# Performance work log

Measured on AMD Instinct MI355X. Metric: run time of the kernel, lower is better.

Reference implementation:

```python
import jax, jax.numpy as jnp
import numpy as np


def setup_inputs() -> dict:
    key = jax.random.key(0)
    ks = jax.random.split(key, 5)
    b, f, h, w, c = 2, 16, 64, 64, 256
    heads, D = 8, 32
    hD = heads * D
    x = jax.random.normal(ks[0], (b, f, h, w, c), dtype=jnp.float32)
    s = 1.0 / np.sqrt(c)
    Wq = jax.random.normal(ks[1], (c, hD), dtype=jnp.float32) * s
    Wk = jax.random.normal(ks[2], (c, hD), dtype=jnp.float32) * s
    Wv = jax.random.normal(ks[3], (c, hD), dtype=jnp.float32) * s
    Wo = jax.random.normal(ks[4], (hD, c), dtype=jnp.float32) * s
    return {"x": x, "Wq": Wq, "Wk": Wk, "Wv": Wv, "Wo": Wo, "heads": heads}


def reference(x, Wq, Wk, Wv, Wo, heads):
    b, f, h, w, c = x.shape
    hD = Wq.shape[1]
    D = hD // heads
    n = h * w
    # fuse batch & frames; 1x1 conv == channel matmul
    xf = x.reshape(b * f, n, c)  # [(bf), n, c]

    def proj(W):
        # [(bf), n, hD] -> [(bf), heads, D, n]
        p = jnp.einsum('bnc,cd->bnd', xf, W)
        return p.reshape(b * f, n, heads, D).transpose(0, 2, 3, 1)

    q = jax.nn.softmax(proj(Wq), axis=-2)  # softmax over D (note: scale is dead code in source)
    k = jax.nn.softmax(proj(Wk), axis=-1)  # softmax over spatial n
    v = proj(Wv)
    context = jnp.einsum('bhdn,bhen->bhde', k, v)      # [(bf), heads, D, D]
    out = jnp.einsum('bhde,bhdn->bhen', context, q)    # [(bf), heads, D, n]
    out = out.transpose(0, 3, 1, 2).reshape(b * f, n, hD)
    out = jnp.einsum('bnd,dc->bnc', out, Wo)
    return out.reshape(b, f, h, w, c)
```

## Files before the change

kernel.cpp:

```cpp
#include <hip/hip_runtime.h>
#include <hip/hip_bf16.h>


typedef __attribute__((ext_vector_type(8))) short bf16x8;
typedef __attribute__((ext_vector_type(4))) float f32x4;

__device__ __forceinline__ unsigned short f2bf(float x) {
  __hip_bfloat16 h = __float2bfloat16(x);
  union { __hip_bfloat16 b; unsigned short u; } c; c.b = h; return c.u;
}

__device__ __forceinline__ void gl16(const unsigned short* g, unsigned short* l) {
  __builtin_amdgcn_global_load_lds((const __attribute__((address_space(1))) void*)g,
                                   (__attribute__((address_space(3))) void*)l, 16, 0, 0);
}

__global__ __launch_bounds__(256) void k0_prep(const float* __restrict__ Wq,
                                               const float* __restrict__ Wk,
                                               const float* __restrict__ Wv,
                                               unsigned short* __restrict__ WqT,
                                               unsigned short* __restrict__ WkvT) {
  int r = blockIdx.x, c = threadIdx.x;
  if (r < 256)      WqT [(r      )*256 + c] = f2bf(Wq[c*256 + r]);
  else if (r < 512) WkvT[(r - 256)*256 + c] = f2bf(Wk[c*256 + (r-256)]);
  else              WkvT[(r - 256)*256 + c] = f2bf(Wv[c*256 + (r-512)]);
}

__global__ __launch_bounds__(1024, 4) void k1w(const float* __restrict__ x,
                                               const unsigned short* __restrict__ WkvT,
                                               float* __restrict__ ctxp,
                                               unsigned short* __restrict__ XB) {
  __shared__ unsigned short As[2][32*256];
  __shared__ unsigned short slab[2][512*32];
  int bid = blockIdx.x;
  size_t rowbase = (size_t)bid * 256;
  int tid = threadIdx.x;
  int lane = tid & 63, w = tid >> 6;
  int cl = lane & 15, rq = (lane >> 4) << 2, fs = lane >> 4;
  int h = w & 7;
  bool isV = w >= 8;

  bf16x8 bfr[2][8];
#pragma unroll
  for (int ni = 0; ni < 2; ++ni)
#pragma unroll
    for (int kk = 0; kk < 8; ++kk)
      bfr[ni][kk] = *(const bf16x8*)(WkvT + (size_t)(w*32 + ni*16 + cl)*256 + kk*32 + fs*8);

  f32x4 c2[2] = {};
  float dena0 = 0.f, dena1 = 0.f;

  int ar = tid >> 5, as_ = tid & 31;
  int aw = ar*256 + ((as_ ^ (ar & 7)) << 3);
  const float* ap = x + (rowbase + ar)*256 + as_*8;
  unsigned short* xbp = XB + (rowbase + ar)*256 + as_*8;

  int ca0 = h*32 + cl, ca1 = h*32 + 16 + cl;
  int cb  = 256 + h*32 + (isV ? 16 : 0) + cl;
  int ra0 = ca0*32 + ((fs ^ ((ca0 ^ (ca0 >> 2)) & 3)) << 3);
  int ra1 = ca1*32 + ((fs ^ ((ca1 ^ (ca1 >> 2)) & 3)) << 3);
  int rb  = cb*32  + ((fs ^ ((cb  ^ (cb  >> 2)) & 3)) << 3);

  f32x4 acc[2][2];

  float4 pa0 = *(const float4*)ap;
  float4 pa1 = *(const float4*)(ap + 4);
  {
    unsigned short* Ab = &As[0][0];
    union { ushort4 u4[2]; int4 i4; } pk;
    pk.u4[0].x = f2bf(pa0.x); pk.u4[0].y = f2bf(pa0.y); pk.u4[0].z = f2bf(pa0.z); pk.u4[0].w = f2bf(pa0.w);
    pk.u4[1].x = f2bf(pa1.x); pk.u4[1].y = f2bf(pa1.y); pk.u4[1].z = f2bf(pa1.z); pk.u4[1].w = f2bf(pa1.w);
    *(int4*)(&Ab[aw]) = pk.i4;
    *(int4*)xbp = pk.i4;
  }
  {
    const float* apn = ap + 32*256;
    pa0 = *(const float4*)apn;
    pa1 = *(const float4*)(apn + 4);
  }
  __syncthreads();
  {
    unsigned short* Ab = &As[0][0];
#pragma unroll
    for (int m = 0; m < 2; ++m)
#pragma unroll
      for (int ni = 0; ni < 2; ++ni) acc[m][ni] = (f32x4){};
#pragma unroll
    for (int kk = 0; kk < 8; ++kk) {
      int so = (((kk*4 + fs) ^ (cl & 7)) << 3);
      bf16x8 a0 = *(const bf16x8*)(&Ab[cl*256 + so]);
      bf16x8 a1 = *(const bf16x8*)(&Ab[(16 + cl)*256 + so]);
#pragma unroll
      for (int ni = 0; ni < 2; ++ni) {
        acc[0][ni] = __builtin_amdgcn_mfma_f32_16x16x32_bf16(a0, bfr[ni][kk], acc[0][ni], 0, 0, 0);
        acc[1][ni] = __builtin_amdgcn_mfma_f32_16x16x32_bf16(a1, bfr[ni][kk], acc[1][ni], 0, 0, 0);
      }
    }
  }

  for (int t = 0; t < 7; ++t) {
    {
      unsigned short* sb = &slab[t & 1][0];
#pragma unroll
      for (int ni = 0; ni < 2; ++ni) {
        int c = w*32 + ni*16 + cl;
        int sw = (c ^ (c >> 2)) & 3;
#pragma unroll
        for (int m = 0; m < 2; ++m) {
          int n4 = m*16 + rq;
          ushort4 wv;
          if (!isV) {
            float e0 = __expf(acc[m][ni][0]), e1 = __expf(acc[m][ni][1]);
            float e2 = __expf(acc[m][ni][2]), e3 = __expf(acc[m][ni][3]);
            if (ni == 0) dena0 += (e0 + e1) + (e2 + e3); else dena1 += (e0 + e1) + (e2 + e3);
            wv.x = f2bf(e0); wv.y = f2bf(e1); wv.z = f2bf(e2); wv.w = f2bf(e3);
          } else {
            wv.x = f2bf(acc[m][ni][0]); wv.y = f2bf(acc[m][ni][1]);
            wv.z = f2bf(acc[m][ni][2]); wv.w = f2bf(acc[m][ni][3]);
          }
          *(ushort4*)(&sb[c*32 + (((n4 >> 3) ^ sw) << 3) + (n4 & 7)]) = wv;
        }
      }
    }
    {
      unsigned short* Ab = &As[(t + 1) & 1][0];
      union { ushort4 u4[2]; int4 i4; } pk;
      pk.u4[0].x = f2bf(pa0.x); pk.u4[0].y = f2bf(pa0.y); pk.u4[0].z = f2bf(pa0.z); pk.u4[0].w = f2bf(pa0.w);
      pk.u4[1].x = f2bf(pa1.x); pk.u4[1].y = f2bf(pa1.y); pk.u4[1].z = f2bf(pa1.z); pk.u4[1].w = f2bf(pa1.w);
      *(int4*)(&Ab[aw]) = pk.i4;
      *(int4*)(xbp + (size_t)(t + 1)*8192) = pk.i4;
    }
    if (t < 6) {
      const float* apn = ap + (size_t)(t + 2)*32*256;
      pa0 = *(const float4*)apn;
      pa1 = *(const float4*)(apn + 4);
    }
    __syncthreads();
    {
      unsigned short* sb = &slab[t & 1][0];
      bf16x8 af0 = *(const bf16x8*)(&sb[ra0]);
      bf16x8 af1 = *(const bf16x8*)(&sb[ra1]);
      bf16x8 bv  = *(const bf16x8*)(&sb[rb]);
      c2[0] = __builtin_amdgcn_mfma_f32_16x16x32_bf16(af0, bv, c2[0], 0, 0, 0);
      c2[1] = __builtin_amdgcn_mfma_f32_16x16x32_bf16(af1, bv, c2[1], 0, 0, 0);
    }
    {
      unsigned short* Ab = &As[(t + 1) & 1][0];
#pragma unroll
      for (int m = 0; m < 2; ++m)
#pragma unroll
        for (int ni = 0; ni < 2; ++ni) acc[m][ni] = (f32x4){};
#pragma unroll
      for (int kk = 0; kk < 8; ++kk) {
        int so = (((kk*4 + fs) ^ (cl & 7)) << 3);
        bf16x8 a0 = *(const bf16x8*)(&Ab[cl*256 + so]);
        bf16x8 a1 = *(const bf16x8*)(&Ab[(16 + cl)*256 + so]);
#pragma unroll
        for (int ni = 0; ni < 2; ++ni) {
          acc[0][ni] = __builtin_amdgcn_mfma_f32_16x16x32_bf16(a0, bfr[ni][kk], acc[0][ni], 0, 0, 0);
          acc[1][ni] = __builtin_amdgcn_mfma_f32_16x16x32_bf16(a1, bfr[ni][kk], acc[1][ni], 0, 0, 0);
        }
      }
    }
  }
  {
    unsigned short* sb = &slab[1][0];
#pragma unroll
    for (int ni = 0; ni < 2; ++ni) {
      int c = w*32 + ni*16 + cl;
      int sw = (c ^ (c >> 2)) & 3;
#pragma unroll
      for (int m = 0; m < 2; ++m) {
        int n4 = m*16 + rq;
        ushort4 wv;
        if (!isV) {
          float e0 = __expf(acc[m][ni][0]), e1 = __expf(acc[m][ni][1]);
          float e2 = __expf(acc[m][ni][2]), e3 = __expf(acc[m][ni][3]);
          if (ni == 0) dena0 += (e0 + e1) + (e2 + e3); else dena1 += (e0 + e1) + (e2 + e3);
          wv.x = f2bf(e0); wv.y = f2bf(e1); wv.z = f2bf(e2); wv.w = f2bf(e3);
        } else {
          wv.x = f2bf(acc[m][ni][0]); wv.y = f2bf(acc[m][ni][1]);
          wv.z = f2bf(acc[m][ni][2]); wv.w = f2bf(acc[m][ni][3]);
        }
        *(ushort4*)(&sb[c*32 + (((n4 >> 3) ^ sw) << 3) + (n4 & 7)]) = wv;
      }
    }
  }
  __syncthreads();
  {
    unsigned short* sb = &slab[1][0];
    bf16x8 af0 = *(const bf16x8*)(&sb[ra0]);
    bf16x8 af1 = *(const bf16x8*)(&sb[ra1]);
    bf16x8 bv  = *(const bf16x8*)(&sb[rb]);
    c2[0] = __builtin_amdgcn_mfma_f32_16x16x32_bf16(af0, bv, c2[0], 0, 0, 0);
    c2[1] = __builtin_amdgcn_mfma_f32_16x16x32_bf16(af1, bv, c2[1], 0, 0, 0);
  }
  float* cp = ctxp + ((size_t)bid*8 + h)*1056;
  int ec = isV ? 16 + cl : cl;
#pragma unroll
  for (int di = 0; di < 2; ++di)
#pragma unroll
    for (int r = 0; r < 4; ++r)
      cp[(di*16 + rq + r)*33 + ec] = c2[di][r];
  if (!isV) {
    dena0 += __shfl_xor(dena0, 16); dena0 += __shfl_xor(dena0, 32);
    dena1 += __shfl_xor(dena1, 16); dena1 += __shfl_xor(dena1, 32);
    if (fs == 0) {
      cp[cl*33 + 32]        = dena0;
      cp[(16 + cl)*33 + 32] = dena1;
    }
  }
}

__global__ __launch_bounds__(256) void k2b_w2(const float* __restrict__ ctxp,
                                              const float* __restrict__ Wo,
                                              unsigned short* __restrict__ W2t) {
  __shared__ float clds[32*33];
  int bid = blockIdx.x;
  int h = bid & 7, bfi = bid >> 3;
  int tid = threadIdx.x;
  for (int i = tid; i < 1056; i += 256) {
    float s = 0.f;
#pragma unroll
    for (int p = 0; p < 16; ++p)
      s += ctxp[((size_t)(bfi*16 + p)*8 + h)*1056 + i];
    clds[i] = s;
  }
  __syncthreads();
  float acc[32] = {};
#pragma unroll 4
  for (int e = 0; e < 32; ++e) {
    float w = Wo[(size_t)(h*32 + e)*256 + tid];
#pragma unroll
    for (int d = 0; d < 32; ++d) acc[d] += clds[d*33 + e] * w;
  }
  unsigned short* o = W2t + ((size_t)bfi*256 + tid)*256 + h*32;
#pragma unroll
  for (int d = 0; d < 32; ++d) o[d] = f2bf(acc[d] / clds[d*33 + 32]);
}

__global__ __launch_bounds__(512, 2) void k3x(const unsigned short* __restrict__ XB,
                                              const unsigned short* __restrict__ WqT,
                                              const unsigned short* __restrict__ W2t,
                                              float* __restrict__ out) {
  __shared__ unsigned short As[2][32*256];
  __shared__ unsigned short Qs[2][32*256];
  int bid = blockIdx.x;
  size_t rowbase = (size_t)bid * 256;
  int bfi = bid >> 4;
  int tid = threadIdx.x;
  int lane = tid & 63, wid = tid >> 6;
  int cl = lane & 15, rq = (lane >> 4) << 2, fs = lane >> 4;

  bf16x8 bq[2][8], bw[2][8];
#pragma unroll
  for (int nf = 0; nf < 2; ++nf)
#pragma unroll
    for (int kk = 0; kk < 8; ++kk) {
      bq[nf][kk] = *(const bf16x8*)(WqT + (size_t)(wid*32 + nf*16 + cl)*256 + kk*32 + fs*8);
      bw[nf][kk] = *(const bf16x8*)(W2t + ((size_t)bfi*256 + wid*32 + nf*16 + cl)*256 + kk*32 + fs*8);
    }

  int sr = tid >> 5, ss = tid & 31;
  const unsigned short* xs0 = XB + (rowbase + sr)*256 + ((ss ^ (sr & 7)) << 3);
  const unsigned short* xs1 = xs0 + 16*256;

  int qslotbase = wid*4 + (rq >> 3);
  ushort4 qpk[2][2];

  auto stageA = [&](int buf, int ts) {
    gl16(xs0 + (size_t)ts*8192, &As[buf][(wid*64)*8]);
    gl16(xs1 + (size_t)ts*8192, &As[buf][(512 + wid*64)*8]);
  };
  auto p1soft = [&](int buf) {
    unsigned short* Ab = &As[buf][0];
    f32x4 ql[2][2] = {};
#pragma unroll
    for (int kk = 0; kk < 8; ++kk) {
      int so = (((kk*4 + fs) ^ (cl & 7)) << 3);
      bf16x8 a0 = *(const bf16x8*)(&Ab[cl*256 + so]);
      bf16x8 a1 = *(const bf16x8*)(&Ab[(16 + cl)*256 + so]);
#pragma unroll
      for (int nf = 0; nf < 2; ++nf) {
        ql[0][nf] = __builtin_amdgcn_mfma_f32_16x16x32_bf16(bq[nf][kk], a0, ql[0][nf], 0, 0, 0);
        ql[1][nf] = __builtin_amdgcn_mfma_f32_16x16x32_bf16(bq[nf][kk], a1, ql[1][nf], 0, 0, 0);
      }
    }
#pragma unroll
    for (int m = 0; m < 2; ++m) {
      float e0[4], e1[4]; float s8 = 0.f;
#pragma unroll
      for (int r = 0; r < 4; ++r) { e0[r] = __expf(ql[m][0][r]); e1[r] = __expf(ql[m][1][r]); s8 += e0[r] + e1[r]; }
      float s = s8; s += __shfl_xor(s, 16); s += __shfl_xor(s, 32);
      float inv = 1.0f / s;
      qpk[m][0].x = f2bf(e0[0]*inv); qpk[m][0].y = f2bf(e0[1]*inv); qpk[m][0].z = f2bf(e0[2]*inv); qpk[m][0].w = f2bf(e0[3]*inv);
      qpk[m][1].x = f2bf(e1[0]*inv); qpk[m][1].y = f2bf(e1[1]*inv); qpk[m][1].z = f2bf(e1[2]*inv); qpk[m][1].w = f2bf(e1[3]*inv);
    }
  };
  auto qwrite = [&](int buf) {
    unsigned short* Qb = &Qs[buf][0];
#pragma unroll
    for (int m = 0; m < 2; ++m) {
      int row = m*16 + cl;
#pragma unroll
      for (int nf = 0; nf < 2; ++nf) {
        int slot = qslotbase + nf*2;
        *(ushort4*)(&Qb[row*256 + ((slot ^ (row & 7)) << 3) + (rq & 4)]) = qpk[m][nf];
      }
    }
  };

  stageA(0, 0);
  __syncthreads();
  p1soft(0);

  for (int t = 0; t < 7; ++t) {
    stageA((t + 1) & 1, t + 1);
    qwrite(t & 1);
    __syncthreads();
    f32x4 oa[2][2] = {};
    {
      unsigned short* Qb = &Qs[t & 1][0];
#pragma unroll
      for (int kk = 0; kk < 8; ++kk) {
        int so = (((kk*4 + fs) ^ (cl & 7)) << 3);
        bf16x8 q0 = *(const bf16x8*)(&Qb[cl*256 + so]);
        bf16x8 q1 = *(const bf16x8*)(&Qb[(16 + cl)*256 + so]);
#pragma unroll
        for (int nf = 0; nf < 2; ++nf) {
          oa[0][nf] = __builtin_amdgcn_mfma_f32_16x16x32_bf16(bw[nf][kk], q0, oa[0][nf], 0, 0, 0);
          oa[1][nf] = __builtin_amdgcn_mfma_f32_16x16x32_bf16(bw[nf][kk], q1, oa[1][nf], 0, 0, 0);
        }
      }
    }
    p1soft((t + 1) & 1);
#pragma unroll
    for (int m = 0; m < 2; ++m)
#pragma unroll
      for (int nf = 0; nf < 2; ++nf)
        *(f32x4*)(&out[(rowbase + (size_t)t*32 + m*16 + cl)*256 + wid*32 + nf*16 + rq]) = oa[m][nf];
  }
  qwrite(1);
  __syncthreads();
  {
    unsigned short* Qb = &Qs[1][0];
    f32x4 oa[2][2] = {};
#pragma unroll
    for (int kk = 0; kk < 8; ++kk) {
      int so = (((kk*4 + fs) ^ (cl & 7)) << 3);
      bf16x8 q0 = *(const bf16x8*)(&Qb[cl*256 + so]);
      bf16x8 q1 = *(const bf16x8*)(&Qb[(16 + cl)*256 + so]);
#pragma unroll
      for (int nf = 0; nf < 2; ++nf) {
        oa[0][nf] = __builtin_amdgcn_mfma_f32_16x16x32_bf16(bw[nf][kk], q0, oa[0][nf], 0, 0, 0);
        oa[1][nf] = __builtin_amdgcn_mfma_f32_16x16x32_bf16(bw[nf][kk], q1, oa[1][nf], 0, 0, 0);
      }
    }
#pragma unroll
    for (int m = 0; m < 2; ++m)
#pragma unroll
      for (int nf = 0; nf < 2; ++nf)
        *(f32x4*)(&out[(rowbase + (size_t)7*32 + m*16 + cl)*256 + wid*32 + nf*16 + rq]) = oa[m][nf];
  }
}

extern "C" void kernel_launch(void* const* d_in, const int* in_sizes, int n_in,
                              void* d_out, int out_size, void* d_ws, size_t ws_size,
                              hipStream_t stream) {
  const float* x  = (const float*)d_in[0];
  const float* Wq = (const float*)d_in[1];
  const float* Wk = (const float*)d_in[2];
  const float* Wv = (const float*)d_in[3];
  const float* Wo = (const float*)d_in[4];
  float* out = (float*)d_out;

  unsigned short* WkvT = (unsigned short*)d_ws;
  unsigned short* WqT  = WkvT + 131072;
  unsigned short* W2t  = WqT  + 65536;
  float*          ctxp = (float*)(W2t + 2097152);
  unsigned short* XB   = (unsigned short*)(ctxp + (size_t)512*8*1056);

  k0_prep <<<768,  256,  0, stream>>>(Wq, Wk, Wv, WqT, WkvT);
  k1w     <<<512,  1024, 0, stream>>>(x, WkvT, ctxp, XB);
  k2b_w2  <<<256,  256,  0, stream>>>(ctxp, Wo, W2t);
  k3x     <<<512,  512,  0, stream>>>(XB, WqT, W2t, out);
}
```

Before: 156.4 us.

## Drop bf16 x staging buffer; reload fp32 x in final kernel and pad slab

The first kernel no longer writes a bf16 copy of x to global memory. The final kernel instead reads fp32 x directly, converts it to bf16 in registers and stores it to LDS, with register prefetch replacing the async global-to-LDS loads. The intent is to remove a 16 MB write and read of the intermediate buffer, at the cost of re-reading 32 MB of fp32 input and doing the conversion work twice. The slab LDS row stride is also padded from 32 to 40, and the prefetch of the next x tile now sits after the barrier.

```diff
diff --git a/kernel.cpp b/kernel.cpp
--- a/kernel.cpp
+++ b/kernel.cpp
@@ -8,11 +8,6 @@
 __device__ __forceinline__ unsigned short f2bf(float x) {
   __hip_bfloat16 h = __float2bfloat16(x);
   union { __hip_bfloat16 b; unsigned short u; } c; c.b = h; return c.u;
-}
-
-__device__ __forceinline__ void gl16(const unsigned short* g, unsigned short* l) {
-  __builtin_amdgcn_global_load_lds((const __attribute__((address_space(1))) void*)g,
-                                   (__attribute__((address_space(3))) void*)l, 16, 0, 0);
 }
 
 __global__ __launch_bounds__(256) void k0_prep(const float* __restrict__ Wq,
@@ -28,10 +23,9 @@
 
 __global__ __launch_bounds__(1024, 4) void k1w(const float* __restrict__ x,
                                                const unsigned short* __restrict__ WkvT,
-                                               float* __restrict__ ctxp,
-                                               unsigned short* __restrict__ XB) {
+                                               float* __restrict__ ctxp) {
   __shared__ unsigned short As[2][32*256];
-  __shared__ unsigned short slab[2][512*32];
+  __shared__ unsigned short slab[2][512*40];
   int bid = blockIdx.x;
   size_t rowbase = (size_t)bid * 256;
   int tid = threadIdx.x;
@@ -53,13 +47,12 @@
   int ar = tid >> 5, as_ = tid & 31;
   int aw = ar*256 + ((as_ ^ (ar & 7)) << 3);
   const float* ap = x + (rowbase + ar)*256 + as_*8;
-  unsigned short* xbp = XB + (rowbase + ar)*256 + as_*8;
 
   int ca0 = h*32 + cl, ca1 = h*32 + 16 + cl;
   int cb  = 256 + h*32 + (isV ? 16 : 0) + cl;
-  int ra0 = ca0*32 + ((fs ^ ((ca0 ^ (ca0 >> 2)) & 3)) << 3);
-  int ra1 = ca1*32 + ((fs ^ ((ca1 ^ (ca1 >> 2)) & 3)) << 3);
-  int rb  = cb*32  + ((fs ^ ((cb  ^ (cb  >> 2)) & 3)) << 3);
+  int ra0 = ca0*40 + ((fs ^ ((ca0 ^ (ca0 >> 2)) & 3)) << 3);
+  int ra1 = ca1*40 + ((fs ^ ((ca1 ^ (ca1 >> 2)) & 3)) << 3);
+  int rb  = cb*40  + ((fs ^ ((cb  ^ (cb  >> 2)) & 3)) << 3);
 
   f32x4 acc[2][2];
 
@@ -71,7 +64,6 @@
     pk.u4[0].x = f2bf(pa0.x); pk.u4[0].y = f2bf(pa0.y); pk.u4[0].z = f2bf(pa0.z); pk.u4[0].w = f2bf(pa0.w);
     pk.u4[1].x = f2bf(pa1.x); pk.u4[1].y = f2bf(pa1.y); pk.u4[1].z = f2bf(pa1.z); pk.u4[1].w = f2bf(pa1.w);
     *(int4*)(&Ab[aw]) = pk.i4;
-    *(int4*)xbp = pk.i4;
   }
   {
     const float* apn = ap + 32*256;
@@ -118,7 +110,7 @@
             wv.x = f2bf(acc[m][ni][0]); wv.y = f2bf(acc[m][ni][1]);
             wv.z = f2bf(acc[m][ni][2]); wv.w = f2bf(acc[m][ni][3]);
           }
-          *(ushort4*)(&sb[c*32 + (((n4 >> 3) ^ sw) << 3) + (n4 & 7)]) = wv;
+          *(ushort4*)(&sb[c*40 + (((n4 >> 3) ^ sw) << 3) + (n4 & 7)]) = wv;
         }
       }
     }
@@ -128,14 +120,13 @@
       pk.u4[0].x = f2bf(pa0.x); pk.u4[0].y = f2bf(pa0.y); pk.u4[0].z = f2bf(pa0.z); pk.u4[0].w = f2bf(pa0.w);
       pk.u4[1].x = f2bf(pa1.x); pk.u4[1].y = f2bf(pa1.y); pk.u4[1].z = f2bf(pa1.z); pk.u4[1].w = f2bf(pa1.w);
       *(int4*)(&Ab[aw]) = pk.i4;
-      *(int4*)(xbp + (size_t)(t + 1)*8192) = pk.i4;
-    }
+    }
+    __syncthreads();
     if (t < 6) {
       const float* apn = ap + (size_t)(t + 2)*32*256;
       pa0 = *(const float4*)apn;
       pa1 = *(const float4*)(apn + 4);
     }
-    __syncthreads();
     {
       unsigned short* sb = &slab[t & 1][0];
       bf16x8 af0 = *(const bf16x8*)(&sb[ra0]);
@@ -182,7 +173,7 @@
           wv.x = f2bf(acc[m][ni][0]); wv.y = f2bf(acc[m][ni][1]);
           wv.z = f2bf(acc[m][ni][2]); wv.w = f2bf(acc[m][ni][3]);
         }
-        *(ushort4*)(&sb[c*32 + (((n4 >> 3) ^ sw) << 3) + (n4 & 7)]) = wv;
+        *(ushort4*)(&sb[c*40 + (((n4 >> 3) ^ sw) << 3) + (n4 & 7)]) = wv;
       }
     }
   }
@@ -239,7 +230,7 @@
   for (int d = 0; d < 32; ++d) o[d] = f2bf(acc[d] / clds[d*33 + 32]);
 }
 
-__global__ __launch_bounds__(512, 2) void k3x(const unsigned short* __restrict__ XB,
+__global__ __launch_bounds__(512, 2) void k3s(const float* __restrict__ x,
                                               const unsigned short* __restrict__ WqT,
                                               const unsigned short* __restrict__ W2t,
                                               float* __restrict__ out) {
@@ -261,16 +252,23 @@
       bw[nf][kk] = *(const bf16x8*)(W2t + ((size_t)bfi*256 + wid*32 + nf*16 + cl)*256 + kk*32 + fs*8);
     }
 
-  int sr = tid >> 5, ss = tid & 31;
-  const unsigned short* xs0 = XB + (rowbase + sr)*256 + ((ss ^ (sr & 7)) << 3);
-  const unsigned short* xs1 = xs0 + 16*256;
+  int ar = tid >> 5, as_ = tid & 31;
+  int aw0 = ar*256 + ((as_ ^ (ar & 7)) << 3);
+  int aw1 = (16 + ar)*256 + ((as_ ^ (ar & 7)) << 3);
+  const float* ap = x + (rowbase + ar)*256 + as_*8;
 
   int qslotbase = wid*4 + (rq >> 3);
   ushort4 qpk[2][2];
 
-  auto stageA = [&](int buf, int ts) {
-    gl16(xs0 + (size_t)ts*8192, &As[buf][(wid*64)*8]);
-    gl16(xs1 + (size_t)ts*8192, &As[buf][(512 + wid*64)*8]);
+  auto stageA = [&](int buf, float4 v0, float4 v1, float4 v2, float4 v3) {
+    unsigned short* Ab = &As[buf][0];
+    union { ushort4 u4[2]; int4 i4; } pk;
+    pk.u4[0].x = f2bf(v0.x); pk.u4[0].y = f2bf(v0.y); pk.u4[0].z = f2bf(v0.z); pk.u4[0].w = f2bf(v0.w);
+    pk.u4[1].x = f2bf(v1.x); pk.u4[1].y = f2bf(v1.y); pk.u4[1].z = f2bf(v1.z); pk.u4[1].w = f2bf(v1.w);
+    *(int4*)(&Ab[aw0]) = pk.i4;
+    pk.u4[0].x = f2bf(v2.x); pk.u4[0].y = f2bf(v2.y); pk.u4[0].z = f2bf(v2.z); pk.u4[0].w = f2bf(v2.w);
+    pk.u4[1].x = f2bf(v3.x); pk.u4[1].y = f2bf(v3.y); pk.u4[1].z = f2bf(v3.z); pk.u4[1].w = f2bf(v3.w);
+    *(int4*)(&Ab[aw1]) = pk.i4;
   };
   auto p1soft = [&](int buf) {
     unsigned short* Ab = &As[buf][0];
@@ -310,14 +308,32 @@
     }
   };
 
-  stageA(0, 0);
+  float4 pa0 = *(const float4*)ap;
+  float4 pa1 = *(const float4*)(ap + 4);
+  float4 pa2 = *(const float4*)(ap + 16*256);
+  float4 pa3 = *(const float4*)(ap + 16*256 + 4);
+  stageA(0, pa0, pa1, pa2, pa3);
+  {
+    const float* apn = ap + 32*256;
+    pa0 = *(const float4*)apn;
+    pa1 = *(const float4*)(apn + 4);
+    pa2 = *(const float4*)(apn + 16*256);
+    pa3 = *(const float4*)(apn + 16*256 + 4);
+  }
   __syncthreads();
   p1soft(0);
 
   for (int t = 0; t < 7; ++t) {
-    stageA((t + 1) & 1, t + 1);
+    stageA((t + 1) & 1, pa0, pa1, pa2, pa3);
     qwrite(t & 1);
     __syncthreads();
+    if (t < 6) {
+      const float* apn = ap + (size_t)(t + 2)*32*256;
+      pa0 = *(const float4*)apn;
+      pa1 = *(const float4*)(apn + 4);
+      pa2 = *(const float4*)(apn + 16*256);
+      pa3 = *(const float4*)(apn + 16*256 + 4);
+    }
     f32x4 oa[2][2] = {};
     {
       unsigned short* Qb = &Qs[t & 1][0];
@@ -378,10 +394,9 @@
   unsigned short* WqT  = WkvT + 131072;
   unsigned short* W2t  = WqT  + 65536;
   float*          ctxp = (float*)(W2t + 2097152);
-  unsigned short* XB   = (unsigned short*)(ctxp + (size_t)512*8*1056);
 
   k0_prep <<<768,  256,  0, stream>>>(Wq, Wk, Wv, WqT, WkvT);
-  k1w     <<<512,  1024, 0, stream>>>(x, WkvT, ctxp, XB);
+  k1w     <<<512,  1024, 0, stream>>>(x, WkvT, ctxp);
   k2b_w2  <<<256,  256,  0, stream>>>(ctxp, Wo, W2t);
-  k3x     <<<512,  512,  0, stream>>>(XB, WqT, W2t, out);
-}
+  k3s     <<<512,  512,  0, stream>>>(x, WqT, W2t, out);
+}
```

New measurement: 143.6 us. -8.1%, faster.
